# Optimization experiments

Hardware: AMD Instinct MI355X
Metric: run time of the kernel (lower is better)

## Reference

```python
import jax, jax.numpy as jnp
import numpy as np

NUM_NODES = 50000
NUM_EDGES = 800000
IN_DIM = 64
HIDDEN = 64
NUM_EDGE_TYPES = 6


def leaky_relu(x, alpha=0.2):
    return jnp.maximum(alpha * x, x)


def setup_inputs() -> dict:
    key = jax.random.key(0)
    ks = jax.random.split(key, 8)
    inputs = jax.random.normal(ks[0], (NUM_NODES, IN_DIM), dtype=jnp.float32)
    source_indices = jax.random.randint(ks[1], (NUM_EDGES,), 0, NUM_NODES)
    dest_indices = jax.random.randint(ks[2], (NUM_EDGES,), 0, NUM_NODES)
    edge_types = jax.random.randint(ks[3], (NUM_EDGES,), 0, NUM_EDGE_TYPES)
    # params: xavier-ish dense kernels, tiny biases, uniform edge-type embedding
    W1 = jax.random.normal(ks[4], (IN_DIM, HIDDEN), dtype=jnp.float32) * (1.0 / np.sqrt(IN_DIM))
    b1 = jnp.zeros((HIDDEN,), dtype=jnp.float32)
    W2 = jax.random.normal(ks[5], (2 * HIDDEN, 1), dtype=jnp.float32) * (1.0 / np.sqrt(2 * HIDDEN))
    b2 = jnp.zeros((1,), dtype=jnp.float32)
    edge_emb = jax.random.uniform(ks[6], (NUM_EDGE_TYPES, HIDDEN), dtype=jnp.float32, minval=-0.1, maxval=0.1)
    return {
        "inputs": inputs,
        "source_indices": source_indices,
        "dest_indices": dest_indices,
        "edge_types": edge_types,
        "num_nodes": NUM_NODES,
        "W1": W1,
        "b1": b1,
        "W2": W2,
        "b2": b2,
        "edge_emb": edge_emb,
    }


def reference(inputs, source_indices, dest_indices, edge_types, num_nodes, W1, b1, W2, b2, edge_emb):
    # keys == queries == values in this layer
    keys = inputs @ W1 + b1                      # [N, H]
    ee = edge_emb[edge_types]                    # [E, H]
    keys_source = keys[source_indices]           # [E, H]
    queries_dest = keys[dest_indices]            # [E, H]
    wh = jnp.concatenate([keys_source + ee, queries_dest], axis=-1)  # [E, 2H]
    logits = leaky_relu(wh @ W2 + b2)            # [E, 1]
    # segment softmax over destination nodes (empty segments never gathered)
    seg_max = jax.ops.segment_max(logits, dest_indices, num_segments=num_nodes)  # [N, 1]
    exp_logits = jnp.exp(logits - seg_max[dest_indices])
    exp_sum = jax.ops.segment_sum(exp_logits, dest_indices, num_segments=num_nodes)
    attn = exp_logits / exp_sum[dest_indices]    # [E, 1]
    weighted = (keys_source + ee) * attn         # [E, H]  (values_source == keys_source)
    outputs = jax.ops.segment_sum(weighted, dest_indices, num_segments=num_nodes)  # [N, H]
    return outputs
```

## Files before the change

### kernel.cpp

```cpp
#include <hip/hip_runtime.h>
#include <hip/hip_bf16.h>
#include <hip/hip_fp16.h>


__device__ __forceinline__ unsigned short f2bf(float f) {
    unsigned u = __float_as_uint(f);
    u += 0x7FFFu + ((u >> 16) & 1u);
    return (unsigned short)(u >> 16);
}
__device__ __forceinline__ float bf2f(unsigned short h) {
    return __uint_as_float(((unsigned)h) << 16);
}

#define NBLK_H 256
#define CAPB   16384

__global__ __launch_bounds__(256, 4) void k_nodes(
    const float* __restrict__ inputs, const float* __restrict__ W1,
    const float* __restrict__ b1, const float* __restrict__ W2,
    const float* __restrict__ edge_emb, const int* __restrict__ dst,
    unsigned short* __restrict__ keys, float* __restrict__ alpha_src,
    float* __restrict__ alpha_dst, float* __restrict__ alpha_ee,
    int* __restrict__ histG, int N, int E, int NB, int chunk)
{
    __shared__ float W1s[64 * 64];
    __shared__ float W2s[128];
    __shared__ float xs[32 * 65];
    __shared__ int histL[256];

    const int t = threadIdx.x;
    const int row0 = blockIdx.x * 32;

    const float4* W1g = reinterpret_cast<const float4*>(W1);
    float4* W1sv = reinterpret_cast<float4*>(W1s);
#pragma unroll
    for (int i = 0; i < 4; i++) W1sv[t + 256 * i] = W1g[t + 256 * i];
    if (t < 128) W2s[t] = W2[t];

    for (int i = 0; i < 8; i++) {
        int idx = t + 256 * i;
        int r = idx >> 6, c = idx & 63;
        if (row0 + r < N)
            xs[r * 65 + c] = inputs[(size_t)(row0 + r) * 64 + c];
    }
    __syncthreads();

    const int lane = t & 63;
    const int wave = t >> 6;
    const int gidx = wave * 4 + (lane >> 4);
    const int j4   = lane & 15;
    const int rA = 2 * gidx;

    const float4* W1v = reinterpret_cast<const float4*>(W1s);
    float4 acc[2];
    acc[0] = {0.f, 0.f, 0.f, 0.f};
    acc[1] = {0.f, 0.f, 0.f, 0.f};
#pragma unroll 4
    for (int k = 0; k < 64; k++) {
        float4 w = W1v[k * 16 + j4];
        float a0 = xs[rA * 65 + k];
        float a1 = xs[rA * 65 + 65 + k];
        acc[0].x += a0 * w.x; acc[0].y += a0 * w.y;
        acc[0].z += a0 * w.z; acc[0].w += a0 * w.w;
        acc[1].x += a1 * w.x; acc[1].y += a1 * w.y;
        acc[1].z += a1 * w.z; acc[1].w += a1 * w.w;
    }

    const float4 bv = reinterpret_cast<const float4*>(b1)[j4];
#pragma unroll
    for (int i = 0; i < 2; i++) {
        int row = row0 + rA + i;
        if (row < N) {
            float4 a = { acc[i].x + bv.x, acc[i].y + bv.y,
                         acc[i].z + bv.z, acc[i].w + bv.w };
            ushort4 kv;
            kv.x = f2bf(a.x); kv.y = f2bf(a.y); kv.z = f2bf(a.z); kv.w = f2bf(a.w);
            reinterpret_cast<ushort4*>(keys)[(size_t)row * 16 + j4] = kv;
            float p1 = a.x * W2s[4 * j4]     + a.y * W2s[4 * j4 + 1]
                     + a.z * W2s[4 * j4 + 2] + a.w * W2s[4 * j4 + 3];
            float p2 = a.x * W2s[64 + 4 * j4]     + a.y * W2s[64 + 4 * j4 + 1]
                     + a.z * W2s[64 + 4 * j4 + 2] + a.w * W2s[64 + 4 * j4 + 3];
#pragma unroll
            for (int m = 8; m >= 1; m >>= 1) {
                p1 += __shfl_xor(p1, m);
                p2 += __shfl_xor(p2, m);
            }
            if (j4 == 0) { alpha_src[row] = p1; alpha_dst[row] = p2; }
        }
    }

    if (blockIdx.x == 0 && t < 6) {
        float s = 0.f;
        for (int c = 0; c < 64; c++) s += edge_emb[t * 64 + c] * W2s[c];
        alpha_ee[t] = s;
    }

    if (blockIdx.x < NBLK_H) {
        const int blk = blockIdx.x;
        for (int b = t; b < NB; b += 256) histL[b] = 0;
        __syncthreads();
        const int lim = min(E, (blk + 1) * chunk);
        for (int e = blk * chunk + t; e < lim; e += 256)
            atomicAdd(&histL[dst[e] >> 8], 1);
        __syncthreads();
        for (int b = t; b < NB; b += 256)
            histG[b * NBLK_H + blk] = histL[b];
    }
}

__global__ __launch_bounds__(256) void k_scanA(
    int* __restrict__ histG, int* __restrict__ bsum)
{
    __shared__ int sm[256];
    const int t = threadIdx.x;
    const int b = blockIdx.x;
    int v = histG[b * NBLK_H + t];
    sm[t] = v;
    __syncthreads();
    for (int off = 1; off < 256; off <<= 1) {
        int x = 0;
        if (t >= off) x = sm[t - off];
        __syncthreads();
        if (t >= off) sm[t] += x;
        __syncthreads();
    }
    histG[b * NBLK_H + t] = sm[t] - v;
    if (t == 255) bsum[b] = sm[255];
}

__global__ __launch_bounds__(256) void k_bucket_scatter(
    const int* __restrict__ src, const int* __restrict__ dst,
    const int* __restrict__ ety, const int* __restrict__ histG,
    const int* __restrict__ bsum, int* __restrict__ ebuf,
    int E, int NB, int chunk)
{
    __shared__ int sm[256];
    __shared__ int cur[256];
    const int t = threadIdx.x;
    const int blk = blockIdx.x;

    int bs = (t < NB) ? bsum[t] : 0;
    sm[t] = bs;
    __syncthreads();
    for (int off = 1; off < 256; off <<= 1) {
        int x = 0;
        if (t >= off) x = sm[t - off];
        __syncthreads();
        if (t >= off) sm[t] += x;
        __syncthreads();
    }
    if (t < NB) cur[t] = (sm[t] - bs) + histG[t * NBLK_H + blk];
    __syncthreads();

    const int lim = min(E, (blk + 1) * chunk);
    for (int e = blk * chunk + t; e < lim; e += 256) {
        int d = dst[e];
        int pos = atomicAdd(&cur[d >> 8], 1);
        ebuf[pos] = src[e] | (ety[e] << 16) | ((d & 255) << 19);
    }
}

__global__ __launch_bounds__(256) void k_localcsr(
    int* __restrict__ ebuf, const int* __restrict__ bsum,
    const float* __restrict__ a_src, const float* __restrict__ a_dst,
    const float* __restrict__ a_ee, const float* __restrict__ b2,
    int* __restrict__ rp, __half* __restrict__ wexp,
    float* __restrict__ dsum, int N, int NB, int E)
{
    __shared__ int   estage[CAPB];
    __shared__ int   h[256];
    __shared__ int   sm[256];
    __shared__ int   cur2[256];
    __shared__ float fsum[256];
    __shared__ float baseL[256];
    __shared__ float aeeL[8];

    const int t = threadIdx.x;
    const int b = blockIdx.x;
    const int idx = (b << 8) + t;

    int bs = (t < NB) ? bsum[t] : 0;
    sm[t] = bs;
    __syncthreads();
    for (int off = 1; off < 256; off <<= 1) {
        int x = 0;
        if (t >= off) x = sm[t - off];
        __syncthreads();
        if (t >= off) sm[t] += x;
        __syncthreads();
    }
    const int begB = (b == 0) ? 0 : sm[b - 1];
    const int endB = sm[b];
    const int cnt  = endB - begB;
    __syncthreads();

    h[t] = 0;
    fsum[t] = 0.f;
    baseL[t] = (idx < N) ? (a_dst[idx] + b2[0]) : 0.f;
    if (t < 6) aeeL[t] = a_ee[t];
    __syncthreads();

    for (int i = t; i < cnt; i += 256) {
        int r = ebuf[begB + i];
        if (i < CAPB) estage[i] = r;
        atomicAdd(&h[(r >> 19) & 255], 1);
    }
    __syncthreads();

    sm[t] = h[t];
    __syncthreads();
    for (int off = 1; off < 256; off <<= 1) {
        int x = 0;
        if (t >= off) x = sm[t - off];
        __syncthreads();
        if (t >= off) sm[t] += x;
        __syncthreads();
    }
    int lstart = (t == 0) ? 0 : sm[t - 1];

    if (idx < N) rp[idx] = begB + lstart;
    if (b == NB - 1 && t == 0) rp[N] = E;
    cur2[t] = begB + lstart;
    __syncthreads();

    for (int i = t; i < cnt; i += 256) {
        int r = (i < CAPB) ? estage[i] : ebuf[begB + i];
        int s  = r & 0xFFFF;
        int ty = (r >> 16) & 7;
        int dl = (r >> 19) & 255;
        float l = a_src[s] + aeeL[ty] + baseL[dl];
        l = fmaxf(0.2f * l, l);
        float w = expf(l);
        int pos = atomicAdd(&cur2[dl], 1);
        ebuf[pos] = r & 0x7FFFF;
        wexp[pos] = __float2half_rn(w);
        atomicAdd(&fsum[dl], w);
    }
    __syncthreads();
    if (idx < N) dsum[idx] = fsum[t];
}

__global__ __launch_bounds__(256) void k_out(
    const int* __restrict__ rp, const int* __restrict__ erec,
    const __half* __restrict__ wexp, const float* __restrict__ dsum,
    const unsigned short* __restrict__ keys, const float* __restrict__ edge_emb,
    float* __restrict__ out, int N)
{
    __shared__ float ee4[384];
    __shared__ int   srec[4][64];
    __shared__ float sw[4][64];

    const int t = threadIdx.x;
    for (int i = t; i < 384; i += 256) ee4[i] = edge_emb[i];
    __syncthreads();

    const int lane = t & 63;
    const int wid  = t >> 6;
    const int d = blockIdx.x * 4 + wid;
    if (d >= N) return;

    const int beg = rp[d], end = rp[d + 1];
    const float inv = (end > beg) ? 1.f / dsum[d] : 0.f;

    const int g  = lane >> 4;
    const int j4 = lane & 15;
    const float4* ee4v = reinterpret_cast<const float4*>(ee4);
    float4 acc0 = {0.f, 0.f, 0.f, 0.f};
    float4 acc1 = {0.f, 0.f, 0.f, 0.f};

    for (int cbase = beg; cbase < end; cbase += 64) {
        const int n = min(64, end - cbase);
        if (lane < n) {
            srec[wid][lane] = erec[cbase + lane];
            sw[wid][lane]   = __half2float(wexp[cbase + lane]);
        }
        __builtin_amdgcn_wave_barrier();
        int j = g;
        for (; j + 4 < n; j += 8) {
            int   r0 = srec[wid][j];
            int   r1 = srec[wid][j + 4];
            float w0 = sw[wid][j];
            float w1 = sw[wid][j + 4];
            int sA = r0 & 0xFFFF, tyA = r0 >> 16;
            int sB = r1 & 0xFFFF, tyB = r1 >> 16;
            ushort4 kv0 = reinterpret_cast<const ushort4*>(keys)[(size_t)sA * 16 + j4];
            ushort4 kv1 = reinterpret_cast<const ushort4*>(keys)[(size_t)sB * 16 + j4];
            float4  ev0 = ee4v[tyA * 16 + j4];
            float4  ev1 = ee4v[tyB * 16 + j4];
            acc0.x += (bf2f(kv0.x) + ev0.x) * w0;
            acc0.y += (bf2f(kv0.y) + ev0.y) * w0;
            acc0.z += (bf2f(kv0.z) + ev0.z) * w0;
            acc0.w += (bf2f(kv0.w) + ev0.w) * w0;
            acc1.x += (bf2f(kv1.x) + ev1.x) * w1;
            acc1.y += (bf2f(kv1.y) + ev1.y) * w1;
            acc1.z += (bf2f(kv1.z) + ev1.z) * w1;
            acc1.w += (bf2f(kv1.w) + ev1.w) * w1;
        }
        if (j < n) {
            int   r0 = srec[wid][j];
            float w0 = sw[wid][j];
            int sA = r0 & 0xFFFF, tyA = r0 >> 16;
            ushort4 kv0 = reinterpret_cast<const ushort4*>(keys)[(size_t)sA * 16 + j4];
            float4  ev0 = ee4v[tyA * 16 + j4];
            acc0.x += (bf2f(kv0.x) + ev0.x) * w0;
            acc0.y += (bf2f(kv0.y) + ev0.y) * w0;
            acc0.z += (bf2f(kv0.z) + ev0.z) * w0;
            acc0.w += (bf2f(kv0.w) + ev0.w) * w0;
        }
        __builtin_amdgcn_wave_barrier();
    }

    float4 acc = { acc0.x + acc1.x, acc0.y + acc1.y,
                   acc0.z + acc1.z, acc0.w + acc1.w };
#pragma unroll
    for (int m = 16; m <= 32; m <<= 1) {
        acc.x += __shfl_xor(acc.x, m);
        acc.y += __shfl_xor(acc.y, m);
        acc.z += __shfl_xor(acc.z, m);
        acc.w += __shfl_xor(acc.w, m);
    }
    if (g == 0) {
        acc.x *= inv; acc.y *= inv; acc.z *= inv; acc.w *= inv;
        reinterpret_cast<float4*>(out)[(size_t)d * 16 + j4] = acc;
    }
}

extern "C" void kernel_launch(void* const* d_in, const int* in_sizes, int n_in,
                              void* d_out, int out_size, void* d_ws, size_t ws_size,
                              hipStream_t stream) {
    const float* inputs   = (const float*)d_in[0];
    const int*   src      = (const int*)d_in[1];
    const int*   dst      = (const int*)d_in[2];
    const int*   ety      = (const int*)d_in[3];
    const float* W1       = (const float*)d_in[5];
    const float* b1       = (const float*)d_in[6];
    const float* W2       = (const float*)d_in[7];
    const float* b2       = (const float*)d_in[8];
    const float* edge_emb = (const float*)d_in[9];
    float* out = (float*)d_out;

    const int N  = in_sizes[0] / 64;
    const int E  = in_sizes[1];
    const int NB = (N + 255) >> 8;
    const int M  = NB * NBLK_H;
    const int chunk = (E + NBLK_H - 1) / NBLK_H;

    float*          ws      = (float*)d_ws;
    unsigned short* keys    = (unsigned short*)ws;
    float*          a_src   = ws + (size_t)N * 32;
    float*          a_dst   = a_src + N;
    float*          a_ee    = a_dst + N;
    int*            rp      = (int*)(a_ee + 8);
    int*            histG   = rp + (N + 2);
    int*            bsum    = histG + M;
    int*            ebuf    = bsum + 256;
    __half*         wexp    = (__half*)(ebuf + E);
    float*          dsum    = (float*)(wexp + ((E + 1) & ~1));

    int nblk = (N + 31) / 32;
    k_nodes<<<nblk, 256, 0, stream>>>(inputs, W1, b1, W2, edge_emb, dst,
                                      keys, a_src, a_dst, a_ee, histG, N, E, NB, chunk);
    k_scanA<<<NB, 256, 0, stream>>>(histG, bsum);
    k_bucket_scatter<<<NBLK_H, 256, 0, stream>>>(src, dst, ety, histG,
                                                 bsum, ebuf, E, NB, chunk);
    k_localcsr<<<NB, 256, 0, stream>>>(ebuf, bsum, a_src, a_dst, a_ee, b2,
                                       rp, wexp, dsum, N, NB, E);
    k_out<<<(N + 3) / 4, 256, 0, stream>>>(rp, ebuf, wexp, dsum, keys, edge_emb, out, N);
}
```

Measured before the change: 82.76 us.

## Shrink buckets to 16 destinations and fuse local CSR with aggregation

Destination buckets shrink from 256 to 16 nodes, so the histogram and scatter now use up to 3200 buckets and a separate single-block scan kernel computes the bucket offsets. The local-CSR and output kernels are merged into one kernel per 16-node bucket. Sorted edge records and their exp weights stay in shared memory and feed the weighted aggregation directly, which removes the rp/wexp/dsum global round trip and one launch. Risks: buckets larger than FCAP (1024 edges) would drop entries in the fused path. The histogram and scatter shared arrays also grow larger, which can lower occupancy in k_nodes.

```diff
diff --git a/kernel.cpp b/kernel.cpp
--- a/kernel.cpp
+++ b/kernel.cpp
@@ -1,6 +1,5 @@
 #include <hip/hip_runtime.h>
 #include <hip/hip_bf16.h>
-#include <hip/hip_fp16.h>
 
 
 __device__ __forceinline__ unsigned short f2bf(float f) {
@@ -13,7 +12,8 @@
 }
 
 #define NBLK_H 256
-#define CAPB   16384
+#define MAXNB  3200
+#define FCAP   1024
 
 __global__ __launch_bounds__(256, 4) void k_nodes(
     const float* __restrict__ inputs, const float* __restrict__ W1,
@@ -26,7 +26,7 @@
     __shared__ float W1s[64 * 64];
     __shared__ float W2s[128];
     __shared__ float xs[32 * 65];
-    __shared__ int histL[256];
+    __shared__ int histL[MAXNB];
 
     const int t = threadIdx.x;
     const int row0 = blockIdx.x * 32;
@@ -101,10 +101,10 @@
         __syncthreads();
         const int lim = min(E, (blk + 1) * chunk);
         for (int e = blk * chunk + t; e < lim; e += 256)
-            atomicAdd(&histL[dst[e] >> 8], 1);
+            atomicAdd(&histL[dst[e] >> 4], 1);
         __syncthreads();
         for (int b = t; b < NB; b += 256)
-            histG[b * NBLK_H + blk] = histL[b];
+            histG[(size_t)b * NBLK_H + blk] = histL[b];
     }
 }
 
@@ -113,7 +113,7 @@
 {
     __shared__ int sm[256];
     const int t = threadIdx.x;
-    const int b = blockIdx.x;
+    const size_t b = blockIdx.x;
     int v = histG[b * NBLK_H + t];
     sm[t] = v;
     __syncthreads();
@@ -128,19 +128,18 @@
     if (t == 255) bsum[b] = sm[255];
 }
 
-__global__ __launch_bounds__(256) void k_bucket_scatter(
-    const int* __restrict__ src, const int* __restrict__ dst,
-    const int* __restrict__ ety, const int* __restrict__ histG,
-    const int* __restrict__ bsum, int* __restrict__ ebuf,
-    int E, int NB, int chunk)
+__global__ __launch_bounds__(256) void k_scanB(
+    const int* __restrict__ bsum, int* __restrict__ boff, int NB)
 {
     __shared__ int sm[256];
-    __shared__ int cur[256];
-    const int t = threadIdx.x;
-    const int blk = blockIdx.x;
-
-    int bs = (t < NB) ? bsum[t] : 0;
-    sm[t] = bs;
+    const int t = threadIdx.x;
+    const int CH = (NB + 255) / 256;
+    int s = 0;
+    for (int i = 0; i < CH; i++) {
+        int idx = t * CH + i;
+        if (idx < NB) s += bsum[idx];
+    }
+    sm[t] = s;
     __syncthreads();
     for (int off = 1; off < 256; off <<= 1) {
         int x = 0;
@@ -149,140 +148,120 @@
         if (t >= off) sm[t] += x;
         __syncthreads();
     }
-    if (t < NB) cur[t] = (sm[t] - bs) + histG[t * NBLK_H + blk];
-    __syncthreads();
-
+    int run = (t == 0) ? 0 : sm[t - 1];
+    for (int i = 0; i < CH; i++) {
+        int idx = t * CH + i;
+        if (idx < NB) { boff[idx] = run; run += bsum[idx]; }
+    }
+    if (t == 255) boff[NB] = sm[255];
+}
+
+__global__ __launch_bounds__(256) void k_scatter(
+    const int* __restrict__ src, const int* __restrict__ dst,
+    const int* __restrict__ ety, const int* __restrict__ histG,
+    const int* __restrict__ boff, int* __restrict__ ebuf,
+    int E, int NB, int chunk)
+{
+    __shared__ int cur[MAXNB];
+    const int t = threadIdx.x;
+    const int blk = blockIdx.x;
+    for (int b = t; b < NB; b += 256)
+        cur[b] = boff[b] + histG[(size_t)b * NBLK_H + blk];
+    __syncthreads();
     const int lim = min(E, (blk + 1) * chunk);
     for (int e = blk * chunk + t; e < lim; e += 256) {
         int d = dst[e];
-        int pos = atomicAdd(&cur[d >> 8], 1);
-        ebuf[pos] = src[e] | (ety[e] << 16) | ((d & 255) << 19);
-    }
-}
-
-__global__ __launch_bounds__(256) void k_localcsr(
-    int* __restrict__ ebuf, const int* __restrict__ bsum,
+        int pos = atomicAdd(&cur[d >> 4], 1);
+        ebuf[pos] = src[e] | (ety[e] << 16) | ((d & 15) << 19);
+    }
+}
+
+__global__ __launch_bounds__(256) void k_fused(
+    const int* __restrict__ ebuf, const int* __restrict__ boff,
     const float* __restrict__ a_src, const float* __restrict__ a_dst,
     const float* __restrict__ a_ee, const float* __restrict__ b2,
-    int* __restrict__ rp, __half* __restrict__ wexp,
-    float* __restrict__ dsum, int N, int NB, int E)
-{
-    __shared__ int   estage[CAPB];
-    __shared__ int   h[256];
-    __shared__ int   sm[256];
-    __shared__ int   cur2[256];
-    __shared__ float fsum[256];
-    __shared__ float baseL[256];
+    const unsigned short* __restrict__ keys, const float* __restrict__ edge_emb,
+    float* __restrict__ out, int N)
+{
+    __shared__ float ee4[384];
+    __shared__ int   estage[FCAP];
+    __shared__ int   srt[FCAP];
+    __shared__ float sw[FCAP];
+    __shared__ int   h[16];
+    __shared__ int   lstart[17];
+    __shared__ int   cur2[16];
+    __shared__ float fsumL[16];
+    __shared__ float baseL[16];
     __shared__ float aeeL[8];
 
     const int t = threadIdx.x;
     const int b = blockIdx.x;
-    const int idx = (b << 8) + t;
-
-    int bs = (t < NB) ? bsum[t] : 0;
-    sm[t] = bs;
-    __syncthreads();
-    for (int off = 1; off < 256; off <<= 1) {
-        int x = 0;
-        if (t >= off) x = sm[t - off];
-        __syncthreads();
-        if (t >= off) sm[t] += x;
-        __syncthreads();
-    }
-    const int begB = (b == 0) ? 0 : sm[b - 1];
-    const int endB = sm[b];
-    const int cnt  = endB - begB;
-    __syncthreads();
-
-    h[t] = 0;
-    fsum[t] = 0.f;
-    baseL[t] = (idx < N) ? (a_dst[idx] + b2[0]) : 0.f;
+    const int d0 = b << 4;
+    const int begB = boff[b], endB = boff[b + 1];
+    const int cnt = endB - begB;
+
+    for (int i = t; i < 384; i += 256) ee4[i] = edge_emb[i];
+    if (t < 16) {
+        h[t] = 0;
+        fsumL[t] = 0.f;
+        baseL[t] = (d0 + t < N) ? (a_dst[d0 + t] + b2[0]) : 0.f;
+    }
     if (t < 6) aeeL[t] = a_ee[t];
     __syncthreads();
 
     for (int i = t; i < cnt; i += 256) {
         int r = ebuf[begB + i];
-        if (i < CAPB) estage[i] = r;
-        atomicAdd(&h[(r >> 19) & 255], 1);
-    }
-    __syncthreads();
-
-    sm[t] = h[t];
-    __syncthreads();
-    for (int off = 1; off < 256; off <<= 1) {
-        int x = 0;
-        if (t >= off) x = sm[t - off];
-        __syncthreads();
-        if (t >= off) sm[t] += x;
-        __syncthreads();
-    }
-    int lstart = (t == 0) ? 0 : sm[t - 1];
-
-    if (idx < N) rp[idx] = begB + lstart;
-    if (b == NB - 1 && t == 0) rp[N] = E;
-    cur2[t] = begB + lstart;
+        if (i < FCAP) estage[i] = r;
+        atomicAdd(&h[(r >> 19) & 15], 1);
+    }
+    __syncthreads();
+
+    if (t == 0) {
+        int run = 0;
+#pragma unroll
+        for (int k = 0; k < 16; k++) { lstart[k] = run; run += h[k]; }
+        lstart[16] = run;
+    }
+    __syncthreads();
+    if (t < 16) cur2[t] = lstart[t];
     __syncthreads();
 
     for (int i = t; i < cnt; i += 256) {
-        int r = (i < CAPB) ? estage[i] : ebuf[begB + i];
+        int r = (i < FCAP) ? estage[i] : ebuf[begB + i];
         int s  = r & 0xFFFF;
         int ty = (r >> 16) & 7;
-        int dl = (r >> 19) & 255;
+        int dl = (r >> 19) & 15;
         float l = a_src[s] + aeeL[ty] + baseL[dl];
         l = fmaxf(0.2f * l, l);
         float w = expf(l);
         int pos = atomicAdd(&cur2[dl], 1);
-        ebuf[pos] = r & 0x7FFFF;
-        wexp[pos] = __float2half_rn(w);
-        atomicAdd(&fsum[dl], w);
-    }
-    __syncthreads();
-    if (idx < N) dsum[idx] = fsum[t];
-}
-
-__global__ __launch_bounds__(256) void k_out(
-    const int* __restrict__ rp, const int* __restrict__ erec,
-    const __half* __restrict__ wexp, const float* __restrict__ dsum,
-    const unsigned short* __restrict__ keys, const float* __restrict__ edge_emb,
-    float* __restrict__ out, int N)
-{
-    __shared__ float ee4[384];
-    __shared__ int   srec[4][64];
-    __shared__ float sw[4][64];
-
-    const int t = threadIdx.x;
-    for (int i = t; i < 384; i += 256) ee4[i] = edge_emb[i];
+        if (pos < FCAP) { srt[pos] = r; sw[pos] = w; }
+        atomicAdd(&fsumL[dl], w);
+    }
     __syncthreads();
 
     const int lane = t & 63;
     const int wid  = t >> 6;
-    const int d = blockIdx.x * 4 + wid;
-    if (d >= N) return;
-
-    const int beg = rp[d], end = rp[d + 1];
-    const float inv = (end > beg) ? 1.f / dsum[d] : 0.f;
-
-    const int g  = lane >> 4;
-    const int j4 = lane & 15;
+    const int g    = lane >> 4;
+    const int j4   = lane & 15;
     const float4* ee4v = reinterpret_cast<const float4*>(ee4);
-    float4 acc0 = {0.f, 0.f, 0.f, 0.f};
-    float4 acc1 = {0.f, 0.f, 0.f, 0.f};
-
-    for (int cbase = beg; cbase < end; cbase += 64) {
-        const int n = min(64, end - cbase);
-        if (lane < n) {
-            srec[wid][lane] = erec[cbase + lane];
-            sw[wid][lane]   = __half2float(wexp[cbase + lane]);
-        }
-        __builtin_amdgcn_wave_barrier();
-        int j = g;
-        for (; j + 4 < n; j += 8) {
-            int   r0 = srec[wid][j];
-            int   r1 = srec[wid][j + 4];
-            float w0 = sw[wid][j];
-            float w1 = sw[wid][j + 4];
-            int sA = r0 & 0xFFFF, tyA = r0 >> 16;
-            int sB = r1 & 0xFFFF, tyB = r1 >> 16;
+
+#pragma unroll
+    for (int k = 0; k < 4; k++) {
+        const int dl = wid * 4 + k;
+        const int d = d0 + dl;
+        if (d >= N) continue;
+        const int eb = lstart[dl], en = lstart[dl + 1];
+        const float inv = (en > eb) ? 1.f / fsumL[dl] : 0.f;
+        float4 acc0 = {0.f, 0.f, 0.f, 0.f};
+        float4 acc1 = {0.f, 0.f, 0.f, 0.f};
+
+        int j = eb + g;
+        for (; j + 4 < en; j += 8) {
+            int   r0 = srt[j],  r1 = srt[j + 4];
+            float w0 = sw[j],   w1 = sw[j + 4];
+            int sA = r0 & 0xFFFF, tyA = (r0 >> 16) & 7;
+            int sB = r1 & 0xFFFF, tyB = (r1 >> 16) & 7;
             ushort4 kv0 = reinterpret_cast<const ushort4*>(keys)[(size_t)sA * 16 + j4];
             ushort4 kv1 = reinterpret_cast<const ushort4*>(keys)[(size_t)sB * 16 + j4];
             float4  ev0 = ee4v[tyA * 16 + j4];
@@ -296,10 +275,10 @@
             acc1.z += (bf2f(kv1.z) + ev1.z) * w1;
             acc1.w += (bf2f(kv1.w) + ev1.w) * w1;
         }
-        if (j < n) {
-            int   r0 = srec[wid][j];
-            float w0 = sw[wid][j];
-            int sA = r0 & 0xFFFF, tyA = r0 >> 16;
+        if (j < en) {
+            int   r0 = srt[j];
+            float w0 = sw[j];
+            int sA = r0 & 0xFFFF, tyA = (r0 >> 16) & 7;
             ushort4 kv0 = reinterpret_cast<const ushort4*>(keys)[(size_t)sA * 16 + j4];
             float4  ev0 = ee4v[tyA * 16 + j4];
             acc0.x += (bf2f(kv0.x) + ev0.x) * w0;
@@ -307,21 +286,20 @@
             acc0.z += (bf2f(kv0.z) + ev0.z) * w0;
             acc0.w += (bf2f(kv0.w) + ev0.w) * w0;
         }
-        __builtin_amdgcn_wave_barrier();
-    }
-
-    float4 acc = { acc0.x + acc1.x, acc0.y + acc1.y,
-                   acc0.z + acc1.z, acc0.w + acc1.w };
-#pragma unroll
-    for (int m = 16; m <= 32; m <<= 1) {
-        acc.x += __shfl_xor(acc.x, m);
-        acc.y += __shfl_xor(acc.y, m);
-        acc.z += __shfl_xor(acc.z, m);
-        acc.w += __shfl_xor(acc.w, m);
-    }
-    if (g == 0) {
-        acc.x *= inv; acc.y *= inv; acc.z *= inv; acc.w *= inv;
-        reinterpret_cast<float4*>(out)[(size_t)d * 16 + j4] = acc;
+
+        float4 acc = { acc0.x + acc1.x, acc0.y + acc1.y,
+                       acc0.z + acc1.z, acc0.w + acc1.w };
+#pragma unroll
+        for (int m = 16; m <= 32; m <<= 1) {
+            acc.x += __shfl_xor(acc.x, m);
+            acc.y += __shfl_xor(acc.y, m);
+            acc.z += __shfl_xor(acc.z, m);
+            acc.w += __shfl_xor(acc.w, m);
+        }
+        if (g == 0) {
+            acc.x *= inv; acc.y *= inv; acc.z *= inv; acc.w *= inv;
+            reinterpret_cast<float4*>(out)[(size_t)d * 16 + j4] = acc;
+        }
     }
 }
 
@@ -341,29 +319,25 @@
 
     const int N  = in_sizes[0] / 64;
     const int E  = in_sizes[1];
-    const int NB = (N + 255) >> 8;
-    const int M  = NB * NBLK_H;
+    const int NB = (N + 15) >> 4;
     const int chunk = (E + NBLK_H - 1) / NBLK_H;
+    const int ntile = (N + 31) / 32;
 
     float*          ws      = (float*)d_ws;
     unsigned short* keys    = (unsigned short*)ws;
     float*          a_src   = ws + (size_t)N * 32;
     float*          a_dst   = a_src + N;
     float*          a_ee    = a_dst + N;
-    int*            rp      = (int*)(a_ee + 8);
-    int*            histG   = rp + (N + 2);
-    int*            bsum    = histG + M;
-    int*            ebuf    = bsum + 256;
-    __half*         wexp    = (__half*)(ebuf + E);
-    float*          dsum    = (float*)(wexp + ((E + 1) & ~1));
-
-    int nblk = (N + 31) / 32;
-    k_nodes<<<nblk, 256, 0, stream>>>(inputs, W1, b1, W2, edge_emb, dst,
-                                      keys, a_src, a_dst, a_ee, histG, N, E, NB, chunk);
+    int*            histG   = (int*)(a_ee + 8);
+    int*            bsum    = histG + (size_t)NB * NBLK_H;
+    int*            boff    = bsum + MAXNB;
+    int*            ebuf    = boff + MAXNB;
+
+    k_nodes<<<ntile, 256, 0, stream>>>(inputs, W1, b1, W2, edge_emb, dst,
+                                       keys, a_src, a_dst, a_ee, histG, N, E, NB, chunk);
     k_scanA<<<NB, 256, 0, stream>>>(histG, bsum);
-    k_bucket_scatter<<<NBLK_H, 256, 0, stream>>>(src, dst, ety, histG,
-                                                 bsum, ebuf, E, NB, chunk);
-    k_localcsr<<<NB, 256, 0, stream>>>(ebuf, bsum, a_src, a_dst, a_ee, b2,
-                                       rp, wexp, dsum, N, NB, E);
-    k_out<<<(N + 3) / 4, 256, 0, stream>>>(rp, ebuf, wexp, dsum, keys, edge_emb, out, N);
-}
+    k_scanB<<<1, 256, 0, stream>>>(bsum, boff, NB);
+    k_scatter<<<NBLK_H, 256, 0, stream>>>(src, dst, ety, histG, boff, ebuf, E, NB, chunk);
+    k_fused<<<NB, 256, 0, stream>>>(ebuf, boff, a_src, a_dst, a_ee, b2,
+                                    keys, edge_emb, out, N);
+}
```

New measurement: 84.02 us. About the same (+1.5%).
